# Kernel optimization log

Measured on AMD Instinct MI355X. Metric: run time of the kernel, lower is better.

The kernel has to match this reference:

```python
import jax, jax.numpy as jnp
import numpy as np
from jax import lax

EPS = 1e-5
DN = ('NCHW', 'OIHW', 'NCHW')


def binarize(x):
    # sign(x) with 0 -> +1, matching _STESign.forward
    return jnp.where(x >= 0, jnp.ones_like(x), -jnp.ones_like(x))


def batchnorm(x, g, b, m, v):
    # inference BatchNorm2d with running stats
    scale = (g / jnp.sqrt(v + EPS))[None, :, None, None]
    shift = (b - m * g / jnp.sqrt(v + EPS))[None, :, None, None]
    return x * scale + shift


def conv(x, w, stride):
    return lax.conv_general_dilated(x, w, (stride, stride), [(1, 1), (1, 1)],
                                    dimension_numbers=DN)


def setup_inputs() -> dict:
    key = jax.random.key(0)
    ks = jax.random.split(key, 24)
    d = {}
    d['x'] = jax.random.normal(ks[0], (32, 3, 224, 224), dtype=jnp.float32)
    d['conv1_w'] = jax.random.normal(ks[1], (32, 3, 3, 3), dtype=jnp.float32) * 0.1
    d['conv2_w'] = jax.random.normal(ks[2], (64, 32, 3, 3), dtype=jnp.float32) * 0.1
    d['conv3_w'] = jax.random.normal(ks[3], (128, 64, 3, 3), dtype=jnp.float32) * 0.1
    d['conv4_w'] = jax.random.normal(ks[4], (256, 128, 3, 3), dtype=jnp.float32) * 0.1
    for i, c in zip(range(1, 5), (32, 64, 128, 256)):
        base = 4 + (i - 1) * 4
        d[f'bn{i}_g'] = jax.random.uniform(ks[base + 1], (c,), dtype=jnp.float32) + 0.5
        d[f'bn{i}_b'] = jax.random.normal(ks[base + 2], (c,), dtype=jnp.float32) * 0.1
        d[f'bn{i}_m'] = jax.random.normal(ks[base + 3], (c,), dtype=jnp.float32) * 0.1
        d[f'bn{i}_v'] = jax.random.uniform(ks[base + 4], (c,), dtype=jnp.float32) + 0.5
    d['fc_w'] = jax.random.normal(ks[21], (2, 256), dtype=jnp.float32) * 0.05
    d['fc_b'] = jnp.zeros((2,), dtype=jnp.float32)
    return d


def reference(x, conv1_w, conv2_w, conv3_w, conv4_w,
              bn1_g, bn1_b, bn1_m, bn1_v,
              bn2_g, bn2_b, bn2_m, bn2_v,
              bn3_g, bn3_b, bn3_m, bn3_v,
              bn4_g, bn4_b, bn4_m, bn4_v,
              fc_w, fc_b):
    # conv1 (real) + bn1
    h = batchnorm(conv(x, conv1_w, 1), bn1_g, bn1_b, bn1_m, bn1_v)
    # BinarizeConv2d: binarize input and weight, then real conv
    h = binarize(batchnorm(conv(binarize(h), binarize(conv2_w), 2), bn2_g, bn2_b, bn2_m, bn2_v))
    h = binarize(batchnorm(conv(binarize(h), binarize(conv3_w), 2), bn3_g, bn3_b, bn3_m, bn3_v))
    h = binarize(batchnorm(conv(binarize(h), binarize(conv4_w), 2), bn4_g, bn4_b, bn4_m, bn4_v))
    # adaptive avg pool to 1x1 -> mean over H,W
    h = jnp.mean(h, axis=(2, 3))  # [B, 256]
    return h @ fc_w.T + fc_b
```

## Files before the change

### kernel.cpp

```cpp
#include <hip/hip_runtime.h>
#include <stdint.h>
#include <math.h>

#define OFF_T2     3712
#define OFF_T3     4224
#define OFF_T4     5248
#define OFF_W2     7296
#define OFF_W3     9600
#define OFF_W4     18816
#define OFF_A1     55680
#define OFF_A2     6478208
#define OFF_A3     9689472
#define OFF_CNT    11295104

#define C2_LW 116
#define C3_LW 58

static __device__ __forceinline__ float2 bnf(float g, float b, float m, float v) {
    float sc = __fdiv_rn(g, __fsqrt_rn(__fadd_rn(v, 1e-5f)));
    float sh = __fsub_rn(b, __fmul_rn(m, sc));
    return make_float2(sc, sh);
}
static __device__ __forceinline__ bool bnpos(float s, float2 p) {
    return __fadd_rn(__fmul_rn(s, p.x), p.y) >= 0.0f;
}
static __device__ __forceinline__ int find_T(int K, float2 p) {
    int lo = -K - 2, hi = K + 2;
    while (lo + 2 < hi) {
        int mid = ((lo + hi) >> 1) & ~1;
        if (bnpos((float)mid, p)) hi = mid; else lo = mid;
    }
    return hi;
}

#define CONV1_BLOCKS 3136
#define PREP_BLOCKS  1586

__global__ __launch_bounds__(256) void k_front(
    const float* __restrict__ x, const float* __restrict__ w1,
    const float* __restrict__ g1, const float* __restrict__ b1,
    const float* __restrict__ m1, const float* __restrict__ v1,
    const float* __restrict__ w2, const float* __restrict__ w3, const float* __restrict__ w4,
    const float* g2, const float* b2, const float* m2, const float* v2,
    const float* g3, const float* b3, const float* m3, const float* v3,
    const float* g4, const float* b4, const float* m4, const float* v4,
    uint32_t* __restrict__ A1,
    int* __restrict__ T2, int* __restrict__ T3, int* __restrict__ T4,
    uint32_t* __restrict__ W2, uint64_t* __restrict__ W3, uint64_t* __restrict__ W4)
{
    int tid = threadIdx.x;
    if (blockIdx.x >= CONV1_BLOCKS) {
        int gtid = (blockIdx.x - CONV1_BLOCKS) * 256 + tid;
        int wid  = gtid >> 6;
        int lane = gtid & 63;
        if (wid < 576) {
            int oc = wid / 9, t = wid - oc * 9;
            float v = (lane < 32) ? w2[oc * 288 + lane * 9 + t] : -1.0f;
            uint64_t m = __ballot(v >= 0.0f);
            if (lane == 0) W2[wid] = (uint32_t)m;
        } else if (wid < 1728) {
            int i = wid - 576;
            int oc = i / 9, t = i - oc * 9;
            float v = w3[oc * 576 + lane * 9 + t];
            uint64_t m = __ballot(v >= 0.0f);
            if (lane == 0) W3[i] = m;
        } else if (wid < 6336) {
            int i = wid - 1728;
            int oc = i / 18, rem = i - oc * 18;
            int t = rem >> 1, h = rem & 1;
            float v = w4[oc * 1152 + (h * 64 + lane) * 9 + t];
            uint64_t m = __ballot(v >= 0.0f);
            if (lane == 0) W4[i] = m;
        } else {
            int c = (wid - 6336) * 64 + lane;
            if (c < 64) {
                T2[c] = find_T(288, bnf(g2[c], b2[c], m2[c], v2[c]));
            } else if (c < 192) {
                int cc = c - 64;
                T3[cc] = find_T(576, bnf(g3[cc], b3[cc], m3[cc], v3[cc]));
            } else if (c < 448) {
                int cc = c - 192;
                T4[cc] = find_T(1152, bnf(g4[cc], b4[cc], m4[cc], v4[cc]));
            }
        }
        return;
    }

    __shared__ float  wl[27 * 32];
    __shared__ float2 s1[32];
    for (int i = tid; i < 864; i += 256) {
        int k = i >> 5, oc = i & 31;
        wl[i] = w1[oc * 27 + k];
    }
    if (tid < 32) s1[tid] = bnf(g1[tid], b1[tid], m1[tid], v1[tid]);
    __syncthreads();

    int idx = blockIdx.x * 256 + tid;
    int xp = idx % 112;
    int t  = idx / 112;
    int y  = t % 224;
    int b  = t / 224;
    int xc = xp * 2;

    const float* xb = x + (size_t)b * 150528;
    float xin[3][3][4];
    if ((unsigned)(y - 1) < 222u && (unsigned)(xp - 1) < 110u) {
        #pragma unroll
        for (int ic = 0; ic < 3; ic++)
            #pragma unroll
            for (int ky = 0; ky < 3; ky++) {
                const float* rp = xb + ic * 50176 + (y - 1 + ky) * 224 + (xc - 1);
                #pragma unroll
                for (int cx = 0; cx < 4; cx++) xin[ic][ky][cx] = rp[cx];
            }
    } else {
        #pragma unroll
        for (int ic = 0; ic < 3; ic++)
            #pragma unroll
            for (int ky = 0; ky < 3; ky++)
                #pragma unroll
                for (int cx = 0; cx < 4; cx++) {
                    int iy = y - 1 + ky, ix = xc - 1 + cx;
                    float v = 0.0f;
                    if ((unsigned)iy < 224u && (unsigned)ix < 224u)
                        v = xb[ic * 50176 + iy * 224 + ix];
                    xin[ic][ky][cx] = v;
                }
    }

    float acc0[32], acc1[32];
    #pragma unroll
    for (int oc = 0; oc < 32; oc++) { acc0[oc] = 0.0f; acc1[oc] = 0.0f; }

    const float4* wl4 = (const float4*)wl;
    #pragma unroll
    for (int k = 0; k < 27; k++) {
        int ic = k / 9, r = (k % 9) / 3, c = k % 3;
        float a0 = xin[ic][r][c];
        float a1 = xin[ic][r][c + 1];
        #pragma unroll
        for (int g8 = 0; g8 < 8; g8++) {
            float4 w = wl4[k * 8 + g8];
            acc0[g8*4+0] = fmaf(a0, w.x, acc0[g8*4+0]);
            acc0[g8*4+1] = fmaf(a0, w.y, acc0[g8*4+1]);
            acc0[g8*4+2] = fmaf(a0, w.z, acc0[g8*4+2]);
            acc0[g8*4+3] = fmaf(a0, w.w, acc0[g8*4+3]);
            acc1[g8*4+0] = fmaf(a1, w.x, acc1[g8*4+0]);
            acc1[g8*4+1] = fmaf(a1, w.y, acc1[g8*4+1]);
            acc1[g8*4+2] = fmaf(a1, w.z, acc1[g8*4+2]);
            acc1[g8*4+3] = fmaf(a1, w.w, acc1[g8*4+3]);
        }
    }

    uint32_t bits0 = 0, bits1 = 0;
    #pragma unroll
    for (int oc = 0; oc < 32; oc++) {
        float2 p = s1[oc];
        bits0 |= (uint32_t)bnpos(acc0[oc], p) << oc;
        bits1 |= (uint32_t)bnpos(acc1[oc], p) << oc;
    }
    uint2* dst = (uint2*)(A1 + (size_t)b * 50176 + y * 224 + xc);
    *dst = make_uint2(bits0, bits1);
}

template<unsigned VM>
static __device__ __forceinline__ bool pred2(const uint32_t (&w)[3][9], int j,
                                             const uint32_t (&wr)[9], int T) {
    int pc = 0;
    #pragma unroll
    for (int ky = 0; ky < 3; ky++)
        #pragma unroll
        for (int kx = 0; kx < 3; kx++) {
            int ti = ky * 3 + kx;
            if (VM & (1u << ti)) pc += __popc(w[ky][2 * j + kx] ^ wr[ti]);
        }
    constexpr int nv = __builtin_popcount(VM);
    return pc <= ((32 * nv - T) >> 1);
}

template<unsigned VM0, unsigned VM>
static __device__ __forceinline__ void group2(const uint32_t* lrow, int g,
        const uint32_t (&wr)[9], int T, uint64_t* dst, int lane) {
    uint32_t win[3][9];
    int c0 = 8 * g;
    #pragma unroll
    for (int r = 0; r < 3; r++) {
        const uint32_t* rp = lrow + r * C2_LW + c0;
        uint4 a = *(const uint4*)(rp);
        uint4 b = *(const uint4*)(rp + 4);
        win[r][0] = a.x; win[r][1] = a.y; win[r][2] = a.z; win[r][3] = a.w;
        win[r][4] = b.x; win[r][5] = b.y; win[r][6] = b.z; win[r][7] = b.w;
        win[r][8] = rp[8];
    }
    uint64_t b0 = __ballot(pred2<VM0>(win, 0, wr, T));
    uint64_t b1 = __ballot(pred2<VM >(win, 1, wr, T));
    uint64_t b2 = __ballot(pred2<VM >(win, 2, wr, T));
    uint64_t b3 = __ballot(pred2<VM >(win, 3, wr, T));
    if (lane == 0) {
        ulonglong2* d = (ulonglong2*)(dst + 4 * g);
        d[0] = make_ulonglong2(b0, b1);
        d[1] = make_ulonglong2(b2, b3);
    }
}

__global__ __launch_bounds__(256) void k_conv2(
    const uint32_t* __restrict__ A1, const uint32_t* __restrict__ W2g,
    const int* __restrict__ T2, uint64_t* __restrict__ A2)
{
    __shared__ __align__(16) uint32_t lds[9 * C2_LW];
    int bi = blockIdx.x;
    int b = bi / 56, rem = bi % 56;
    int oyq = rem >> 1, h = rem & 1;
    int xs = h * 56;
    int tid = threadIdx.x;
    const uint32_t* ap = A1 + (size_t)b * 50176;
    for (int i = tid; i < 9 * C2_LW; i += 256) {
        int r = i / C2_LW, c = i - r * C2_LW;
        int iy = oyq * 8 - 1 + r, ix = 2 * xs - 1 + c;
        uint32_t v = 0;
        if ((unsigned)iy < 224u && (unsigned)ix < 224u) v = ap[iy * 224 + ix];
        lds[i] = v;
    }
    __syncthreads();

    int w = tid >> 6, lane = tid & 63;
    int oy = oyq * 4 + w;
    uint32_t wr[9];
    #pragma unroll
    for (int ti = 0; ti < 9; ti++) wr[ti] = W2g[lane * 9 + ti];
    int T = T2[lane];
    const uint32_t* lrow = lds + 2 * w * C2_LW;
    uint64_t* dst = A2 + (size_t)b * 12544 + oy * 112 + xs;
    bool left = (xs == 0);

    if (oy == 0) {
        if (left) group2<0x1B0, 0x1F8>(lrow, 0, wr, T, dst, lane);
        else      group2<0x1F8, 0x1F8>(lrow, 0, wr, T, dst, lane);
        for (int g = 1; g < 14; g++) group2<0x1F8, 0x1F8>(lrow, g, wr, T, dst, lane);
    } else {
        if (left) group2<0x1B6, 0x1FF>(lrow, 0, wr, T, dst, lane);
        else      group2<0x1FF, 0x1FF>(lrow, 0, wr, T, dst, lane);
        for (int g = 1; g < 14; g++) group2<0x1FF, 0x1FF>(lrow, g, wr, T, dst, lane);
    }
}

template<unsigned VM>
static __device__ __forceinline__ bool pred3(const uint64_t (&w)[3][9], int j,
                                             const uint64_t (&wr)[9], int T) {
    int pc = 0;
    #pragma unroll
    for (int ky = 0; ky < 3; ky++)
        #pragma unroll
        for (int kx = 0; kx < 3; kx++) {
            int ti = ky * 3 + kx;
            if (VM & (1u << ti)) pc += __popcll(w[ky][2 * j + kx] ^ wr[ti]);
        }
    constexpr int nv = __builtin_popcount(VM);
    return pc <= ((64 * nv - T) >> 1);
}

template<unsigned VM0, unsigned VM>
static __device__ __forceinline__ void group3(const uint64_t* lrow, int g,
        const uint64_t (&wr)[9], int T, uint64_t* dst, int lane) {
    uint64_t win[3][9];
    int c0 = 8 * g;
    #pragma unroll
    for (int r = 0; r < 3; r++) {
        const uint64_t* rp = lrow + r * C3_LW + c0;
        ulonglong2 a0 = *(const ulonglong2*)(rp);
        ulonglong2 a1 = *(const ulonglong2*)(rp + 2);
        ulonglong2 a2 = *(const ulonglong2*)(rp + 4);
        ulonglong2 a3 = *(const ulonglong2*)(rp + 6);
        win[r][0] = a0.x; win[r][1] = a0.y; win[r][2] = a1.x; win[r][3] = a1.y;
        win[r][4] = a2.x; win[r][5] = a2.y; win[r][6] = a3.x; win[r][7] = a3.y;
        win[r][8] = rp[8];
    }
    uint64_t b0 = __ballot(pred3<VM0>(win, 0, wr, T));
    uint64_t b1 = __ballot(pred3<VM >(win, 1, wr, T));
    uint64_t b2 = __ballot(pred3<VM >(win, 2, wr, T));
    uint64_t b3 = __ballot(pred3<VM >(win, 3, wr, T));
    if (lane == 0) {
        ulonglong2* d = (ulonglong2*)(dst + 4 * g);
        d[0] = make_ulonglong2(b0, b1);
        d[1] = make_ulonglong2(b2, b3);
    }
}

__global__ __launch_bounds__(256) void k_conv3(
    const uint64_t* __restrict__ A2, const uint64_t* __restrict__ W3g,
    const int* __restrict__ T3, uint64_t* __restrict__ A3)
{
    __shared__ __align__(16) uint64_t lds[5 * C3_LW];
    int bi = blockIdx.x;
    int b = bi / 56, rem = bi % 56;
    int oyp = rem >> 1, h = rem & 1;
    int xs = h * 28;
    int tid = threadIdx.x;
    const uint64_t* ap = A2 + (size_t)b * 12544;
    for (int i = tid; i < 5 * C3_LW; i += 256) {
        int r = i / C3_LW, c = i - r * C3_LW;
        int iy = oyp * 4 - 1 + r, ix = 2 * xs - 1 + c;
        uint64_t v = 0;
        if ((unsigned)iy < 112u && (unsigned)ix < 112u) v = ap[iy * 112 + ix];
        lds[i] = v;
    }
    __syncthreads();

    int w = tid >> 6, lane = tid & 63;
    int oy = oyp * 2 + (w >> 1);
    int g  = w & 1;
    int oc = g * 64 + lane;
    uint64_t wr[9];
    #pragma unroll
    for (int ti = 0; ti < 9; ti++) wr[ti] = W3g[oc * 9 + ti];
    int T = T3[oc];
    const uint64_t* lrow = lds + 2 * (w >> 1) * C3_LW;
    uint64_t* dst = A3 + (size_t)g * 100352 + (size_t)b * 3136 + oy * 56 + xs;
    bool left = (xs == 0);

    if (oy == 0) {
        if (left) group3<0x1B0, 0x1F8>(lrow, 0, wr, T, dst, lane);
        else      group3<0x1F8, 0x1F8>(lrow, 0, wr, T, dst, lane);
        for (int gg = 1; gg < 7; gg++) group3<0x1F8, 0x1F8>(lrow, gg, wr, T, dst, lane);
    } else {
        if (left) group3<0x1B6, 0x1FF>(lrow, 0, wr, T, dst, lane);
        else      group3<0x1FF, 0x1FF>(lrow, 0, wr, T, dst, lane);
        for (int gg = 1; gg < 7; gg++) group3<0x1FF, 0x1FF>(lrow, gg, wr, T, dst, lane);
    }
}

template<unsigned VM>
static __device__ __forceinline__ bool pred4(const uint64_t (&w0)[3][5],
                                             const uint64_t (&w1)[3][5], int j,
                                             const ulonglong2 (&wr)[9], int T) {
    int pc = 0;
    #pragma unroll
    for (int ky = 0; ky < 3; ky++)
        #pragma unroll
        for (int kx = 0; kx < 3; kx++) {
            int ti = ky * 3 + kx;
            if (VM & (1u << ti)) {
                pc += __popcll(w0[ky][2 * j + kx] ^ wr[ti].x);
                pc += __popcll(w1[ky][2 * j + kx] ^ wr[ti].y);
            }
        }
    constexpr int nv = __builtin_popcount(VM);
    return pc <= ((128 * nv - T) >> 1);
}

template<unsigned VM0, unsigned VM>
static __device__ __forceinline__ int group4c(const uint64_t* ldsb, int g,
        const ulonglong2 (&wr)[9], int T) {
    uint64_t w0[3][5], w1[3][5];
    int c0 = 4 * g;
    #pragma unroll
    for (int r = 0; r < 3; r++) {
        const uint64_t* rp0 = ldsb + r * 30 + c0;
        const uint64_t* rp1 = ldsb + (3 + r) * 30 + c0;
        ulonglong2 a0 = *(const ulonglong2*)(rp0);
        ulonglong2 a1 = *(const ulonglong2*)(rp0 + 2);
        w0[r][0] = a0.x; w0[r][1] = a0.y; w0[r][2] = a1.x; w0[r][3] = a1.y;
        w0[r][4] = rp0[4];
        ulonglong2 b0 = *(const ulonglong2*)(rp1);
        ulonglong2 b1 = *(const ulonglong2*)(rp1 + 2);
        w1[r][0] = b0.x; w1[r][1] = b0.y; w1[r][2] = b1.x; w1[r][3] = b1.y;
        w1[r][4] = rp1[4];
    }
    int c = 0;
    c += pred4<VM0>(w0, w1, 0, wr, T) ? 1 : 0;
    c += pred4<VM >(w0, w1, 1, wr, T) ? 1 : 0;
    return c;
}

__global__ __launch_bounds__(256) void k_conv4(
    const uint64_t* __restrict__ A3, const uint64_t* __restrict__ W4g,
    const int* __restrict__ T4, int* __restrict__ CNT)
{
    __shared__ __align__(16) uint64_t lds[2 * 3 * 30];
    int bi = blockIdx.x;
    int b = bi / 56, rem = bi % 56;
    int oy = rem >> 1, h = rem & 1;
    int tid = threadIdx.x;
    const uint64_t* ap = A3 + (size_t)b * 3136;
    for (int i = tid; i < 174; i += 256) {
        int p = i / 87, j = i - p * 87;
        int r = j / 29, c = j - r * 29;
        int iy = 2 * oy - 1 + r, ix = 2 * h * 14 - 1 + c;
        uint64_t v = 0;
        if ((unsigned)iy < 56u && (unsigned)ix < 56u)
            v = ap[(size_t)p * 100352 + iy * 56 + ix];
        lds[(p * 3 + r) * 30 + c] = v;
    }
    __syncthreads();

    int w = tid >> 6, lane = tid & 63;
    int oc = w * 64 + lane;
    ulonglong2 wr[9];
    const ulonglong2* wp = (const ulonglong2*)(W4g + oc * 18);
    #pragma unroll
    for (int ti = 0; ti < 9; ti++) wr[ti] = wp[ti];
    int T = T4[oc];
    bool left = (h == 0);

    int cnt = 0;
    if (oy == 0) {
        if (left) cnt += group4c<0x1B0, 0x1F8>(lds, 0, wr, T);
        else      cnt += group4c<0x1F8, 0x1F8>(lds, 0, wr, T);
        for (int g = 1; g < 7; g++) cnt += group4c<0x1F8, 0x1F8>(lds, g, wr, T);
    } else {
        if (left) cnt += group4c<0x1B6, 0x1FF>(lds, 0, wr, T);
        else      cnt += group4c<0x1FF, 0x1FF>(lds, 0, wr, T);
        for (int g = 1; g < 7; g++) cnt += group4c<0x1FF, 0x1FF>(lds, g, wr, T);
    }
    atomicAdd(&CNT[b * 256 + oc], cnt);
}

__global__ __launch_bounds__(256) void k_tail(
    const int* __restrict__ CNT, const float* __restrict__ fcw,
    const float* __restrict__ fcb, float* __restrict__ out)
{
    int b = blockIdx.x;
    int c = threadIdx.x;
    int cnt = CNT[b * 256 + c];
    double mean = (2.0 * (double)cnt - 784.0) * (1.0 / 784.0);

    __shared__ double r0[256], r1[256];
    r0[c] = (double)fcw[c]       * mean;
    r1[c] = (double)fcw[256 + c] * mean;
    __syncthreads();
    for (int s = 128; s > 0; s >>= 1) {
        if (c < s) { r0[c] += r0[c + s]; r1[c] += r1[c + s]; }
        __syncthreads();
    }
    if (c == 0) {
        out[b * 2 + 0] = (float)(r0[0] + (double)fcb[0]);
        out[b * 2 + 1] = (float)(r1[0] + (double)fcb[1]);
    }
}

extern "C" void kernel_launch(void* const* d_in, const int* in_sizes, int n_in,
                              void* d_out, int out_size, void* d_ws, size_t ws_size,
                              hipStream_t stream) {
    const float* x   = (const float*)d_in[0];
    const float* w1  = (const float*)d_in[1];
    const float* w2  = (const float*)d_in[2];
    const float* w3  = (const float*)d_in[3];
    const float* w4  = (const float*)d_in[4];
    const float* g1 = (const float*)d_in[5],  *b1 = (const float*)d_in[6],
               * m1 = (const float*)d_in[7],  *v1 = (const float*)d_in[8];
    const float* g2 = (const float*)d_in[9],  *b2 = (const float*)d_in[10],
               * m2 = (const float*)d_in[11], *v2 = (const float*)d_in[12];
    const float* g3 = (const float*)d_in[13], *b3 = (const float*)d_in[14],
               * m3 = (const float*)d_in[15], *v3 = (const float*)d_in[16];
    const float* g4 = (const float*)d_in[17], *b4 = (const float*)d_in[18],
               * m4 = (const float*)d_in[19], *v4 = (const float*)d_in[20];
    const float* fcw = (const float*)d_in[21];
    const float* fcb = (const float*)d_in[22];
    float* out = (float*)d_out;

    char* ws = (char*)d_ws;
    int*      T2  = (int*)(ws + OFF_T2);
    int*      T3  = (int*)(ws + OFF_T3);
    int*      T4  = (int*)(ws + OFF_T4);
    uint32_t* W2  = (uint32_t*)(ws + OFF_W2);
    uint64_t* W3  = (uint64_t*)(ws + OFF_W3);
    uint64_t* W4  = (uint64_t*)(ws + OFF_W4);
    uint32_t* A1  = (uint32_t*)(ws + OFF_A1);
    uint64_t* A2  = (uint64_t*)(ws + OFF_A2);
    uint64_t* A3  = (uint64_t*)(ws + OFF_A3);
    int*      CNT = (int*)(ws + OFF_CNT);

    hipMemsetAsync(CNT, 0, 32 * 256 * sizeof(int), stream);
    hipLaunchKernelGGL(k_front, dim3(CONV1_BLOCKS + PREP_BLOCKS), dim3(256), 0, stream,
                       x, w1, g1, b1, m1, v1, w2, w3, w4,
                       g2, b2, m2, v2, g3, b3, m3, v3, g4, b4, m4, v4,
                       A1, T2, T3, T4, W2, W3, W4);
    hipLaunchKernelGGL(k_conv2, dim3(1792), dim3(256), 0, stream, A1, W2, T2, A2);
    hipLaunchKernelGGL(k_conv3, dim3(1792), dim3(256), 0, stream, A2, W3, T3, A3);
    hipLaunchKernelGGL(k_conv4, dim3(1792), dim3(256), 0, stream, A3, W4, T4, CNT);
    hipLaunchKernelGGL(k_tail,  dim3(32),   dim3(256), 0, stream, CNT, fcw, fcb, out);
}
```

Measured before the change: 217.6 us.

## Fuse conv3, conv4 and FC tail into one tiled kernel; retile conv1

Merges conv3, conv4 and the final FC reduction into a single kernel. Each 1024-thread block loads an A2 tile with halo into LDS, computes the needed conv3 rows (with overlap recompute) into LDS, and then runs conv4 from LDS. A per-batch arrival counter lets the last block finish the FC. The memset is folded into the front kernel, and conv1 now computes 4 pixels × 16 channels per thread, writing 16-bit halves. This removes the A3 global round trip and three launches, but only 256 large blocks are launched and halo rows are recomputed.

```diff
diff --git a/kernel.cpp b/kernel.cpp
--- a/kernel.cpp
+++ b/kernel.cpp
@@ -10,11 +10,10 @@
 #define OFF_W4     18816
 #define OFF_A1     55680
 #define OFF_A2     6478208
-#define OFF_A3     9689472
-#define OFF_CNT    11295104
+#define OFF_CNT    9689472
+#define OFF_ARR    9722240
 
 #define C2_LW 116
-#define C3_LW 58
 
 static __device__ __forceinline__ float2 bnf(float g, float b, float m, float v) {
     float sc = __fdiv_rn(g, __fsqrt_rn(__fadd_rn(v, 1e-5f)));
@@ -34,7 +33,7 @@
 }
 
 #define CONV1_BLOCKS 3136
-#define PREP_BLOCKS  1586
+#define PREP_BLOCKS  1619
 
 __global__ __launch_bounds__(256) void k_front(
     const float* __restrict__ x, const float* __restrict__ w1,
@@ -46,7 +45,8 @@
     const float* g4, const float* b4, const float* m4, const float* v4,
     uint32_t* __restrict__ A1,
     int* __restrict__ T2, int* __restrict__ T3, int* __restrict__ T4,
-    uint32_t* __restrict__ W2, uint64_t* __restrict__ W3, uint64_t* __restrict__ W4)
+    uint32_t* __restrict__ W2, uint64_t* __restrict__ W3, uint64_t* __restrict__ W4,
+    int* __restrict__ Z )
 {
     int tid = threadIdx.x;
     if (blockIdx.x >= CONV1_BLOCKS) {
@@ -71,7 +71,7 @@
             float v = w4[oc * 1152 + (h * 64 + lane) * 9 + t];
             uint64_t m = __ballot(v >= 0.0f);
             if (lane == 0) W4[i] = m;
-        } else {
+        } else if (wid < 6344) {
             int c = (wid - 6336) * 64 + lane;
             if (c < 64) {
                 T2[c] = find_T(288, bnf(g2[c], b2[c], m2[c], v2[c]));
@@ -82,6 +82,9 @@
                 int cc = c - 192;
                 T4[cc] = find_T(1152, bnf(g4[cc], b4[cc], m4[cc], v4[cc]));
             }
+        } else {
+            int zi = gtid - 406016;
+            if (zi < 8256) Z[zi] = 0;
         }
         return;
     }
@@ -95,72 +98,82 @@
     if (tid < 32) s1[tid] = bnf(g1[tid], b1[tid], m1[tid], v1[tid]);
     __syncthreads();
 
-    int idx = blockIdx.x * 256 + tid;
-    int xp = idx % 112;
-    int t  = idx / 112;
+    int half = tid >> 7;
+    int q    = blockIdx.x * 128 + (tid & 127);
+    int xq = q % 56;
+    int t  = q / 56;
     int y  = t % 224;
     int b  = t / 224;
-    int xc = xp * 2;
+    int xc = xq * 4;
 
     const float* xb = x + (size_t)b * 150528;
-    float xin[3][3][4];
-    if ((unsigned)(y - 1) < 222u && (unsigned)(xp - 1) < 110u) {
+    bool interior = ((unsigned)(y - 1) < 222u) && ((unsigned)(xq - 1) < 54u);
+
+    float acc0[16], acc1[16], acc2[16], acc3[16];
+    #pragma unroll
+    for (int i = 0; i < 16; i++) { acc0[i]=0.0f; acc1[i]=0.0f; acc2[i]=0.0f; acc3[i]=0.0f; }
+
+    const float4* wl4 = (const float4*)wl;
+    #pragma unroll
+    for (int ic = 0; ic < 3; ic++)
         #pragma unroll
-        for (int ic = 0; ic < 3; ic++)
+        for (int ky = 0; ky < 3; ky++) {
+            int iy = y - 1 + ky;
+            const float* rp = xb + ic * 50176 + iy * 224 + (xc - 1);
+            float r[6];
+            if (interior) {
+                #pragma unroll
+                for (int c = 0; c < 6; c++) r[c] = rp[c];
+            } else {
+                #pragma unroll
+                for (int c = 0; c < 6; c++) {
+                    int ix = xc - 1 + c;
+                    r[c] = ((unsigned)iy < 224u && (unsigned)ix < 224u) ? rp[c] : 0.0f;
+                }
+            }
             #pragma unroll
-            for (int ky = 0; ky < 3; ky++) {
-                const float* rp = xb + ic * 50176 + (y - 1 + ky) * 224 + (xc - 1);
+            for (int kx = 0; kx < 3; kx++) {
+                int k = ic * 9 + ky * 3 + kx;
+                float a0 = r[kx], a1 = r[kx+1], a2 = r[kx+2], a3 = r[kx+3];
+                const float4* base = wl4 + k * 8 + half * 4;
                 #pragma unroll
-                for (int cx = 0; cx < 4; cx++) xin[ic][ky][cx] = rp[cx];
-            }
-    } else {
-        #pragma unroll
-        for (int ic = 0; ic < 3; ic++)
-            #pragma unroll
-            for (int ky = 0; ky < 3; ky++)
-                #pragma unroll
-                for (int cx = 0; cx < 4; cx++) {
-                    int iy = y - 1 + ky, ix = xc - 1 + cx;
-                    float v = 0.0f;
-                    if ((unsigned)iy < 224u && (unsigned)ix < 224u)
-                        v = xb[ic * 50176 + iy * 224 + ix];
-                    xin[ic][ky][cx] = v;
+                for (int g4i = 0; g4i < 4; g4i++) {
+                    float4 w = base[g4i];
+                    acc0[g4i*4+0] = fmaf(a0, w.x, acc0[g4i*4+0]);
+                    acc0[g4i*4+1] = fmaf(a0, w.y, acc0[g4i*4+1]);
+                    acc0[g4i*4+2] = fmaf(a0, w.z, acc0[g4i*4+2]);
+                    acc0[g4i*4+3] = fmaf(a0, w.w, acc0[g4i*4+3]);
+                    acc1[g4i*4+0] = fmaf(a1, w.x, acc1[g4i*4+0]);
+                    acc1[g4i*4+1] = fmaf(a1, w.y, acc1[g4i*4+1]);
+                    acc1[g4i*4+2] = fmaf(a1, w.z, acc1[g4i*4+2]);
+                    acc1[g4i*4+3] = fmaf(a1, w.w, acc1[g4i*4+3]);
+                    acc2[g4i*4+0] = fmaf(a2, w.x, acc2[g4i*4+0]);
+                    acc2[g4i*4+1] = fmaf(a2, w.y, acc2[g4i*4+1]);
+                    acc2[g4i*4+2] = fmaf(a2, w.z, acc2[g4i*4+2]);
+                    acc2[g4i*4+3] = fmaf(a2, w.w, acc2[g4i*4+3]);
+                    acc3[g4i*4+0] = fmaf(a3, w.x, acc3[g4i*4+0]);
+                    acc3[g4i*4+1] = fmaf(a3, w.y, acc3[g4i*4+1]);
+                    acc3[g4i*4+2] = fmaf(a3, w.z, acc3[g4i*4+2]);
+                    acc3[g4i*4+3] = fmaf(a3, w.w, acc3[g4i*4+3]);
                 }
-    }
-
-    float acc0[32], acc1[32];
-    #pragma unroll
-    for (int oc = 0; oc < 32; oc++) { acc0[oc] = 0.0f; acc1[oc] = 0.0f; }
-
-    const float4* wl4 = (const float4*)wl;
-    #pragma unroll
-    for (int k = 0; k < 27; k++) {
-        int ic = k / 9, r = (k % 9) / 3, c = k % 3;
-        float a0 = xin[ic][r][c];
-        float a1 = xin[ic][r][c + 1];
-        #pragma unroll
-        for (int g8 = 0; g8 < 8; g8++) {
-            float4 w = wl4[k * 8 + g8];
-            acc0[g8*4+0] = fmaf(a0, w.x, acc0[g8*4+0]);
-            acc0[g8*4+1] = fmaf(a0, w.y, acc0[g8*4+1]);
-            acc0[g8*4+2] = fmaf(a0, w.z, acc0[g8*4+2]);
-            acc0[g8*4+3] = fmaf(a0, w.w, acc0[g8*4+3]);
-            acc1[g8*4+0] = fmaf(a1, w.x, acc1[g8*4+0]);
-            acc1[g8*4+1] = fmaf(a1, w.y, acc1[g8*4+1]);
-            acc1[g8*4+2] = fmaf(a1, w.z, acc1[g8*4+2]);
-            acc1[g8*4+3] = fmaf(a1, w.w, acc1[g8*4+3]);
-        }
-    }
-
-    uint32_t bits0 = 0, bits1 = 0;
-    #pragma unroll
-    for (int oc = 0; oc < 32; oc++) {
-        float2 p = s1[oc];
-        bits0 |= (uint32_t)bnpos(acc0[oc], p) << oc;
-        bits1 |= (uint32_t)bnpos(acc1[oc], p) << oc;
-    }
-    uint2* dst = (uint2*)(A1 + (size_t)b * 50176 + y * 224 + xc);
-    *dst = make_uint2(bits0, bits1);
+            }
+        }
+
+    unsigned bits0 = 0, bits1 = 0, bits2 = 0, bits3 = 0;
+    #pragma unroll
+    for (int i = 0; i < 16; i++) {
+        float2 p = s1[16 * half + i];
+        bits0 |= (unsigned)bnpos(acc0[i], p) << i;
+        bits1 |= (unsigned)bnpos(acc1[i], p) << i;
+        bits2 |= (unsigned)bnpos(acc2[i], p) << i;
+        bits3 |= (unsigned)bnpos(acc3[i], p) << i;
+    }
+    uint16_t* dst = (uint16_t*)A1;
+    size_t pbase = (size_t)b * 50176 + y * 224 + xc;
+    dst[2*(pbase+0)+half] = (uint16_t)bits0;
+    dst[2*(pbase+1)+half] = (uint16_t)bits1;
+    dst[2*(pbase+2)+half] = (uint16_t)bits2;
+    dst[2*(pbase+3)+half] = (uint16_t)bits3;
 }
 
 template<unsigned VM>
@@ -259,14 +272,14 @@
     return pc <= ((64 * nv - T) >> 1);
 }
 
-template<unsigned VM0, unsigned VM>
-static __device__ __forceinline__ void group3(const uint64_t* lrow, int g,
-        const uint64_t (&wr)[9], int T, uint64_t* dst, int lane) {
+#define A2SL 60
+template<unsigned M0, unsigned M1, unsigned M2, unsigned M3>
+static __device__ __forceinline__ void group3v(const uint64_t* lrow, int c0,
+        const uint64_t (&wr)[9], int T, uint64_t* orow, int lane) {
     uint64_t win[3][9];
-    int c0 = 8 * g;
     #pragma unroll
     for (int r = 0; r < 3; r++) {
-        const uint64_t* rp = lrow + r * C3_LW + c0;
+        const uint64_t* rp = lrow + r * A2SL + 2 * c0;
         ulonglong2 a0 = *(const ulonglong2*)(rp);
         ulonglong2 a1 = *(const ulonglong2*)(rp + 2);
         ulonglong2 a2 = *(const ulonglong2*)(rp + 4);
@@ -275,57 +288,14 @@
         win[r][4] = a2.x; win[r][5] = a2.y; win[r][6] = a3.x; win[r][7] = a3.y;
         win[r][8] = rp[8];
     }
-    uint64_t b0 = __ballot(pred3<VM0>(win, 0, wr, T));
-    uint64_t b1 = __ballot(pred3<VM >(win, 1, wr, T));
-    uint64_t b2 = __ballot(pred3<VM >(win, 2, wr, T));
-    uint64_t b3 = __ballot(pred3<VM >(win, 3, wr, T));
+    uint64_t b0 = 0, b1 = 0, b2 = 0, b3 = 0;
+    if constexpr (M0 != 0) b0 = __ballot(pred3<M0>(win, 0, wr, T)); else b0 = 0;
+    if constexpr (M1 != 0) b1 = __ballot(pred3<M1>(win, 1, wr, T)); else b1 = 0;
+    if constexpr (M2 != 0) b2 = __ballot(pred3<M2>(win, 2, wr, T)); else b2 = 0;
+    if constexpr (M3 != 0) b3 = __ballot(pred3<M3>(win, 3, wr, T)); else b3 = 0;
     if (lane == 0) {
-        ulonglong2* d = (ulonglong2*)(dst + 4 * g);
-        d[0] = make_ulonglong2(b0, b1);
-        d[1] = make_ulonglong2(b2, b3);
-    }
-}
-
-__global__ __launch_bounds__(256) void k_conv3(
-    const uint64_t* __restrict__ A2, const uint64_t* __restrict__ W3g,
-    const int* __restrict__ T3, uint64_t* __restrict__ A3)
-{
-    __shared__ __align__(16) uint64_t lds[5 * C3_LW];
-    int bi = blockIdx.x;
-    int b = bi / 56, rem = bi % 56;
-    int oyp = rem >> 1, h = rem & 1;
-    int xs = h * 28;
-    int tid = threadIdx.x;
-    const uint64_t* ap = A2 + (size_t)b * 12544;
-    for (int i = tid; i < 5 * C3_LW; i += 256) {
-        int r = i / C3_LW, c = i - r * C3_LW;
-        int iy = oyp * 4 - 1 + r, ix = 2 * xs - 1 + c;
-        uint64_t v = 0;
-        if ((unsigned)iy < 112u && (unsigned)ix < 112u) v = ap[iy * 112 + ix];
-        lds[i] = v;
-    }
-    __syncthreads();
-
-    int w = tid >> 6, lane = tid & 63;
-    int oy = oyp * 2 + (w >> 1);
-    int g  = w & 1;
-    int oc = g * 64 + lane;
-    uint64_t wr[9];
-    #pragma unroll
-    for (int ti = 0; ti < 9; ti++) wr[ti] = W3g[oc * 9 + ti];
-    int T = T3[oc];
-    const uint64_t* lrow = lds + 2 * (w >> 1) * C3_LW;
-    uint64_t* dst = A3 + (size_t)g * 100352 + (size_t)b * 3136 + oy * 56 + xs;
-    bool left = (xs == 0);
-
-    if (oy == 0) {
-        if (left) group3<0x1B0, 0x1F8>(lrow, 0, wr, T, dst, lane);
-        else      group3<0x1F8, 0x1F8>(lrow, 0, wr, T, dst, lane);
-        for (int gg = 1; gg < 7; gg++) group3<0x1F8, 0x1F8>(lrow, gg, wr, T, dst, lane);
-    } else {
-        if (left) group3<0x1B6, 0x1FF>(lrow, 0, wr, T, dst, lane);
-        else      group3<0x1FF, 0x1FF>(lrow, 0, wr, T, dst, lane);
-        for (int gg = 1; gg < 7; gg++) group3<0x1FF, 0x1FF>(lrow, gg, wr, T, dst, lane);
+        orow[c0 + 0] = b0; orow[c0 + 1] = b1;
+        orow[c0 + 2] = b2; orow[c0 + 3] = b3;
     }
 }
 
@@ -348,15 +318,14 @@
     return pc <= ((128 * nv - T) >> 1);
 }
 
-template<unsigned VM0, unsigned VM>
-static __device__ __forceinline__ int group4c(const uint64_t* ldsb, int g,
+template<unsigned M0, unsigned M1>
+static __device__ __forceinline__ int group4v(const uint64_t* A3s, int r15b, int c0,
         const ulonglong2 (&wr)[9], int T) {
     uint64_t w0[3][5], w1[3][5];
-    int c0 = 4 * g;
     #pragma unroll
     for (int r = 0; r < 3; r++) {
-        const uint64_t* rp0 = ldsb + r * 30 + c0;
-        const uint64_t* rp1 = ldsb + (3 + r) * 30 + c0;
+        const uint64_t* rp0 = A3s + (r15b + r) * 32 + c0;
+        const uint64_t* rp1 = A3s + (480 + (r15b + r) * 32) + c0;
         ulonglong2 a0 = *(const ulonglong2*)(rp0);
         ulonglong2 a1 = *(const ulonglong2*)(rp0 + 2);
         w0[r][0] = a0.x; w0[r][1] = a0.y; w0[r][2] = a1.x; w0[r][3] = a1.y;
@@ -367,74 +336,132 @@
         w1[r][4] = rp1[4];
     }
     int c = 0;
-    c += pred4<VM0>(w0, w1, 0, wr, T) ? 1 : 0;
-    c += pred4<VM >(w0, w1, 1, wr, T) ? 1 : 0;
+    if constexpr (M0 != 0) c += pred4<M0>(w0, w1, 0, wr, T) ? 1 : 0;
+    if constexpr (M1 != 0) c += pred4<M1>(w0, w1, 1, wr, T) ? 1 : 0;
     return c;
 }
 
-__global__ __launch_bounds__(256) void k_conv4(
-    const uint64_t* __restrict__ A3, const uint64_t* __restrict__ W4g,
-    const int* __restrict__ T4, int* __restrict__ CNT)
+__global__ __launch_bounds__(1024) void k_rest(
+    const uint64_t* __restrict__ A2g, const uint64_t* __restrict__ W3g,
+    const int* __restrict__ T3, const uint64_t* __restrict__ W4g,
+    const int* __restrict__ T4, int* __restrict__ CNT, int* __restrict__ ARR,
+    const float* __restrict__ fcw, const float* __restrict__ fcb,
+    float* __restrict__ out)
 {
-    __shared__ __align__(16) uint64_t lds[2 * 3 * 30];
+    __shared__ __align__(16) uint64_t A2s[31 * A2SL];
+    __shared__ __align__(16) uint64_t A3s[2 * 15 * 32];
+    __shared__ int flag;
+
     int bi = blockIdx.x;
-    int b = bi / 56, rem = bi % 56;
-    int oy = rem >> 1, h = rem & 1;
+    int b = bi >> 3, q = (bi >> 1) & 3, h = bi & 1;
     int tid = threadIdx.x;
-    const uint64_t* ap = A3 + (size_t)b * 3136;
-    for (int i = tid; i < 174; i += 256) {
-        int p = i / 87, j = i - p * 87;
-        int r = j / 29, c = j - r * 29;
-        int iy = 2 * oy - 1 + r, ix = 2 * h * 14 - 1 + c;
+    int wv = tid >> 6, lane = tid & 63;
+
+    const uint64_t* ap = A2g + (size_t)b * 12544;
+    for (int i = tid; i < 31 * A2SL; i += 1024) {
+        int rl = i / A2SL, cl = i - rl * A2SL;
+        int y2 = 28 * q - 3 + rl, x2 = 56 * h - 3 + cl;
         uint64_t v = 0;
-        if ((unsigned)iy < 56u && (unsigned)ix < 56u)
-            v = ap[(size_t)p * 100352 + iy * 56 + ix];
-        lds[(p * 3 + r) * 30 + c] = v;
+        if ((unsigned)y2 < 112u && (unsigned)x2 < 112u) v = ap[y2 * 112 + x2];
+        A2s[i] = v;
     }
     __syncthreads();
 
-    int w = tid >> 6, lane = tid & 63;
-    int oc = w * 64 + lane;
-    ulonglong2 wr[9];
-    const ulonglong2* wp = (const ulonglong2*)(W4g + oc * 18);
-    #pragma unroll
-    for (int ti = 0; ti < 9; ti++) wr[ti] = wp[ti];
-    int T = T4[oc];
-    bool left = (h == 0);
-
-    int cnt = 0;
-    if (oy == 0) {
-        if (left) cnt += group4c<0x1B0, 0x1F8>(lds, 0, wr, T);
-        else      cnt += group4c<0x1F8, 0x1F8>(lds, 0, wr, T);
-        for (int g = 1; g < 7; g++) cnt += group4c<0x1F8, 0x1F8>(lds, g, wr, T);
-    } else {
-        if (left) cnt += group4c<0x1B6, 0x1FF>(lds, 0, wr, T);
-        else      cnt += group4c<0x1FF, 0x1FF>(lds, 0, wr, T);
-        for (int g = 1; g < 7; g++) cnt += group4c<0x1FF, 0x1FF>(lds, g, wr, T);
-    }
-    atomicAdd(&CNT[b * 256 + oc], cnt);
-}
-
-__global__ __launch_bounds__(256) void k_tail(
-    const int* __restrict__ CNT, const float* __restrict__ fcw,
-    const float* __restrict__ fcb, float* __restrict__ out)
-{
-    int b = blockIdx.x;
-    int c = threadIdx.x;
-    int cnt = CNT[b * 256 + c];
-    double mean = (2.0 * (double)cnt - 784.0) * (1.0 / 784.0);
-
-    __shared__ double r0[256], r1[256];
-    r0[c] = (double)fcw[c]       * mean;
-    r1[c] = (double)fcw[256 + c] * mean;
+    for (int ti = wv; ti < 30; ti += 16) {
+        int r15 = ti >> 1, g = ti & 1;
+        int y3 = 14 * q - 1 + r15;
+        uint64_t* orow = &A3s[(g * 15 + r15) * 32];
+        if ((unsigned)y3 >= 56u) {
+            if (lane < 32) orow[lane] = 0;
+            continue;
+        }
+        int oc = g * 64 + lane;
+        uint64_t wr[9];
+        #pragma unroll
+        for (int t9 = 0; t9 < 9; t9++) wr[t9] = W3g[oc * 9 + t9];
+        int T = T3[oc];
+        const uint64_t* lrow = A2s + (2 * r15) * A2SL;
+        bool top = (y3 == 0);
+        if (h == 0) {
+            if (top) {
+                group3v<0, 0x1B0, 0x1F8, 0x1F8>(lrow, 0, wr, T, orow, lane);
+                for (int gg = 1; gg < 7; gg++)
+                    group3v<0x1F8, 0x1F8, 0x1F8, 0x1F8>(lrow, 4 * gg, wr, T, orow, lane);
+                group3v<0x1F8, 0x1F8, 0x1F8, 0x1F8>(lrow, 25, wr, T, orow, lane);
+            } else {
+                group3v<0, 0x1B6, 0x1FF, 0x1FF>(lrow, 0, wr, T, orow, lane);
+                for (int gg = 1; gg < 7; gg++)
+                    group3v<0x1FF, 0x1FF, 0x1FF, 0x1FF>(lrow, 4 * gg, wr, T, orow, lane);
+                group3v<0x1FF, 0x1FF, 0x1FF, 0x1FF>(lrow, 25, wr, T, orow, lane);
+            }
+        } else {
+            if (top) {
+                for (int gg = 0; gg < 7; gg++)
+                    group3v<0x1F8, 0x1F8, 0x1F8, 0x1F8>(lrow, 4 * gg, wr, T, orow, lane);
+                group3v<0x1F8, 0x1F8, 0x1F8, 0x1F8>(lrow, 25, wr, T, orow, lane);
+            } else {
+                for (int gg = 0; gg < 7; gg++)
+                    group3v<0x1FF, 0x1FF, 0x1FF, 0x1FF>(lrow, 4 * gg, wr, T, orow, lane);
+                group3v<0x1FF, 0x1FF, 0x1FF, 0x1FF>(lrow, 25, wr, T, orow, lane);
+            }
+        }
+    }
     __syncthreads();
-    for (int s = 128; s > 0; s >>= 1) {
-        if (c < s) { r0[c] += r0[c + s]; r1[c] += r1[c + s]; }
+
+    for (int ti = wv; ti < 28; ti += 16) {
+        int oyL = ti >> 2, g4 = ti & 3;
+        int oy = 7 * q + oyL;
+        int oc = g4 * 64 + lane;
+        ulonglong2 wr[9];
+        const ulonglong2* wp = (const ulonglong2*)(W4g + oc * 18);
+        #pragma unroll
+        for (int t9 = 0; t9 < 9; t9++) wr[t9] = wp[t9];
+        int T = T4[oc];
+        int r15b = 2 * oyL;
+        int cnt = 0;
+        if (oy == 0) {
+            if (h == 0) {
+                cnt += group4v<0x1B0, 0x1F8>(A3s, r15b, 0, wr, T);
+                for (int gg = 1; gg < 7; gg++) cnt += group4v<0x1F8, 0x1F8>(A3s, r15b, 4 * gg, wr, T);
+            } else {
+                for (int gg = 0; gg < 7; gg++) cnt += group4v<0x1F8, 0x1F8>(A3s, r15b, 4 * gg, wr, T);
+            }
+        } else {
+            if (h == 0) {
+                cnt += group4v<0x1B6, 0x1FF>(A3s, r15b, 0, wr, T);
+                for (int gg = 1; gg < 7; gg++) cnt += group4v<0x1FF, 0x1FF>(A3s, r15b, 4 * gg, wr, T);
+            } else {
+                for (int gg = 0; gg < 7; gg++) cnt += group4v<0x1FF, 0x1FF>(A3s, r15b, 4 * gg, wr, T);
+            }
+        }
+        atomicAdd(&CNT[b * 256 + oc], cnt);
+    }
+
+    __syncthreads();
+    if (tid == 0) {
+        __threadfence();
+        flag = atomicAdd(&ARR[b], 1);
+    }
+    __syncthreads();
+    if (flag == 7) {
+        __threadfence();
+        double* r0 = (double*)A2s;
+        double* r1 = r0 + 256;
+        if (tid < 256) {
+            int cnt = atomicAdd(&CNT[b * 256 + tid], 0);
+            double mean = (2.0 * (double)cnt - 784.0) * (1.0 / 784.0);
+            r0[tid] = (double)fcw[tid]       * mean;
+            r1[tid] = (double)fcw[256 + tid] * mean;
+        }
         __syncthreads();
-    }
-    if (c == 0) {
-        out[b * 2 + 0] = (float)(r0[0] + (double)fcb[0]);
-        out[b * 2 + 1] = (float)(r1[0] + (double)fcb[1]);
+        for (int s = 128; s > 0; s >>= 1) {
+            if (tid < s) { r0[tid] += r0[tid + s]; r1[tid] += r1[tid + s]; }
+            __syncthreads();
+        }
+        if (tid == 0) {
+            out[b * 2 + 0] = (float)(r0[0] + (double)fcb[0]);
+            out[b * 2 + 1] = (float)(r1[0] + (double)fcb[1]);
+        }
     }
 }
 
@@ -467,16 +494,14 @@
     uint64_t* W4  = (uint64_t*)(ws + OFF_W4);
     uint32_t* A1  = (uint32_t*)(ws + OFF_A1);
     uint64_t* A2  = (uint64_t*)(ws + OFF_A2);
-    uint64_t* A3  = (uint64_t*)(ws + OFF_A3);
     int*      CNT = (int*)(ws + OFF_CNT);
-
-    hipMemsetAsync(CNT, 0, 32 * 256 * sizeof(int), stream);
+    int*      ARR = (int*)(ws + OFF_ARR);
+
     hipLaunchKernelGGL(k_front, dim3(CONV1_BLOCKS + PREP_BLOCKS), dim3(256), 0, stream,
                        x, w1, g1, b1, m1, v1, w2, w3, w4,
                        g2, b2, m2, v2, g3, b3, m3, v3, g4, b4, m4, v4,
-                       A1, T2, T3, T4, W2, W3, W4);
+                       A1, T2, T3, T4, W2, W3, W4, CNT);
     hipLaunchKernelGGL(k_conv2, dim3(1792), dim3(256), 0, stream, A1, W2, T2, A2);
-    hipLaunchKernelGGL(k_conv3, dim3(1792), dim3(256), 0, stream, A2, W3, T3, A3);
-    hipLaunchKernelGGL(k_conv4, dim3(1792), dim3(256), 0, stream, A3, W4, T4, CNT);
-    hipLaunchKernelGGL(k_tail,  dim3(32),   dim3(256), 0, stream, CNT, fcw, fcb, out);
-}
+    hipLaunchKernelGGL(k_rest,  dim3(256),  dim3(1024), 0, stream,
+                       A2, W3, T3, W4, T4, CNT, ARR, fcw, fcb, out);
+}
```

After: 342.4 us. 1.57x slower.
